# Optimization experiments

Hardware: AMD Instinct MI355X
Metric: run time of the kernel (lower is better)

## Reference

```python
import jax, jax.numpy as jnp
import numpy as np

B, T, D_IN, D_OUT = 4, 2048, 1024, 1024


def setup_inputs() -> dict:
    key = jax.random.key(0)
    k1, k2, k3, k4 = jax.random.split(key, 4)
    s_in = 1.0 / np.sqrt(D_IN)
    return {
        "input_vector": jax.random.normal(k1, (B, T, D_IN), dtype=jnp.float32),
        "w_q": jax.random.normal(k2, (D_IN, D_OUT), dtype=jnp.float32) * s_in,
        "w_k": jax.random.normal(k3, (D_IN, D_OUT), dtype=jnp.float32) * s_in,
        "w_v": jax.random.normal(k4, (D_IN, D_OUT), dtype=jnp.float32) * s_in,
    }


def reference(input_vector, w_q, w_k, w_v):
    # projections: [B, T, D_OUT]
    q = jnp.einsum("btd,de->bte", input_vector, w_q)
    k = jnp.einsum("btd,de->bte", input_vector, w_k)
    v = jnp.einsum("btd,de->bte", input_vector, w_v)

    T_ = q.shape[1]
    # raw scores [B, T, T]
    scores = jnp.einsum("bqd,bkd->bqk", q, k)
    # causal mask (strict upper triangle masked to -inf), applied BEFORE scaling
    # (as in the original; -inf is invariant under the scale anyway)
    causal = jnp.tril(jnp.ones((T_, T_), dtype=bool))  # True = keep
    scores = jnp.where(causal[None, :, :], scores, -jnp.inf)
    scores = scores / jnp.sqrt(jnp.asarray(k.shape[-1], scores.dtype))
    attn = jax.nn.softmax(scores, axis=-1)
    # dropout = 0.0 (eval): identity
    return jnp.einsum("bqk,bkd->bqd", attn, v)
```

## Files before the change

### kernel.cpp

```cpp
#include <hip/hip_runtime.h>
#include <cstdint>
#include <math.h>

typedef unsigned short u16;
typedef __attribute__((ext_vector_type(8))) short short8;
typedef __attribute__((ext_vector_type(16))) float f32x16;

__device__ __forceinline__ u16 f2bf(float f) {
  uint32_t u = __float_as_uint(f);
  u += 0x7FFFu + ((u >> 16) & 1u);
  return (u16)(u >> 16);
}
__device__ __forceinline__ float bf2f(u16 h) {
  return __uint_as_float(((uint32_t)h) << 16);
}

__device__ __forceinline__ void async_ld16(u16* lds, const u16* g) {
  __builtin_amdgcn_global_load_lds((const __attribute__((address_space(1))) uint32_t*)g,
                                   (__attribute__((address_space(3))) uint32_t*)lds,
                                   16, 0, 0);
}

template <bool OUT_BF16, int MODE, bool KLIM>
__global__ __launch_bounds__(256) void gemm_bt(
    const u16* __restrict__ A, int lda, long zsA,
    const u16* __restrict__ B, int ldb, long zsB,
    void* __restrict__ Cv, int ldc, long zsC,
    int K, float scale, int NB)
{
  const int b = blockIdx.x, zb = blockIdx.y;
  int nb, mb;
  if constexpr (MODE == 1) {
    const int u = b & 7, v = b >> 3;
    nb = v & (NB - 1);
    mb = u * ((int)(gridDim.x >> 3) / NB) + (v / NB);
  } else if constexpr (MODE == 2) {
    const int u = b & 7, idx = b >> 3;
    if (idx <= u) { mb = u;      nb = idx; }
    else          { mb = 15 - u; nb = idx - u - 1; }
  } else if constexpr (MODE == 3) {
    const int u = b & 7, idx = b >> 3;
    mb = (idx < 8) ? u : 15 - u;
    nb = idx & 7;
  } else {
    nb = b % NB;
    mb = b / NB;
  }

  A += (long)zb * zsA;
  B += (long)zb * zsB;
  const int m0 = mb * 128, n0 = nb * 128;

  __shared__ __align__(16) u16 lsA[2][128 * 32];
  __shared__ __align__(16) u16 lsB[2][128 * 32];

  const int tid = threadIdx.x;
  const int lane = tid & 63;
  const int wave = tid >> 6;
  const int wr = (wave >> 1) * 64;
  const int wc = (wave & 1) * 64;

  f32x16 acc[2][2];
#pragma unroll
  for (int i = 0; i < 2; ++i)
#pragma unroll
    for (int j = 0; j < 2; ++j)
#pragma unroll
      for (int r = 0; r < 16; ++r) acc[i][j][r] = 0.f;

  const int c0 = tid;
  const int c1 = tid + 256;
  const int r0 = c0 >> 2, q0 = ((c0 & 3) ^ ((c0 >> 3) & 3)) * 8;
  const int r1 = c1 >> 2, q1 = ((c1 & 3) ^ ((c1 >> 3) & 3)) * 8;

  const int klim = (mb + 1) * 128;
  const int kmax = KLIM ? (K < klim ? K : klim) : K;

  const u16* pA0 = A + (long)(m0 + r0) * lda + q0;
  const u16* pA1 = A + (long)(m0 + r1) * lda + q1;
  const u16* pB0 = B + (long)(n0 + r0) * ldb + q0;
  const u16* pB1 = B + (long)(n0 + r1) * ldb + q1;

  const int m32 = lane & 31;
  const int hh = lane >> 5;
  const int rsw = (m32 >> 1) & 3;
  int offA[2][2], offB[2][2];
#pragma unroll
  for (int i = 0; i < 2; ++i)
#pragma unroll
    for (int ks = 0; ks < 2; ++ks) {
      const int kq = ((ks << 1) | hh) ^ rsw;
      offA[i][ks] = (wr + i * 32 + m32) * 32 + kq * 8;
      offB[i][ks] = (wc + i * 32 + m32) * 32 + kq * 8;
    }

  async_ld16(&lsA[0][c0 * 8], pA0);
  async_ld16(&lsA[0][c1 * 8], pA1);
  async_ld16(&lsB[0][c0 * 8], pB0);
  async_ld16(&lsB[0][c1 * 8], pB1);
  pA0 += 32; pA1 += 32; pB0 += 32; pB1 += 32;

  int p = 0;
  for (int k0 = 0; k0 < kmax; k0 += 32) {
    __syncthreads();
    if (k0 + 32 < kmax) {
      async_ld16(&lsA[p ^ 1][c0 * 8], pA0);
      async_ld16(&lsA[p ^ 1][c1 * 8], pA1);
      async_ld16(&lsB[p ^ 1][c0 * 8], pB0);
      async_ld16(&lsB[p ^ 1][c1 * 8], pB1);
      pA0 += 32; pA1 += 32; pB0 += 32; pB1 += 32;
    }

    const u16* la = lsA[p];
    const u16* lb = lsB[p];
#pragma unroll
    for (int ks = 0; ks < 2; ++ks) {
      const short8 a0 = *(const short8*)&la[offA[0][ks]];
      const short8 a1 = *(const short8*)&la[offA[1][ks]];
      const short8 b0 = *(const short8*)&lb[offB[0][ks]];
      const short8 b1 = *(const short8*)&lb[offB[1][ks]];
      acc[0][0] = __builtin_amdgcn_mfma_f32_32x32x16_bf16(a0, b0, acc[0][0], 0, 0, 0);
      acc[0][1] = __builtin_amdgcn_mfma_f32_32x32x16_bf16(a0, b1, acc[0][1], 0, 0, 0);
      acc[1][0] = __builtin_amdgcn_mfma_f32_32x32x16_bf16(a1, b0, acc[1][0], 0, 0, 0);
      acc[1][1] = __builtin_amdgcn_mfma_f32_32x32x16_bf16(a1, b1, acc[1][1], 0, 0, 0);
    }
    p ^= 1;
  }

  const int ec = lane & 31;
  const int rb = (lane >> 5) * 4;

  if constexpr (OUT_BF16) {
    u16* C = (u16*)Cv + (long)zb * zsC;
#pragma unroll
    for (int i = 0; i < 2; ++i) {
      const int rbase = m0 + wr + i * 32 + rb;
#pragma unroll
      for (int j = 0; j < 2; ++j) {
        const int col = n0 + wc + j * 32 + ec;
#pragma unroll
        for (int r = 0; r < 16; ++r) {
          const int row = rbase + (r & 3) + 8 * (r >> 2);
          C[(long)row * ldc + col] = f2bf(acc[i][j][r] * scale);
        }
      }
    }
  } else {
    float* C = (float*)Cv + (long)zb * zsC;
#pragma unroll
    for (int i = 0; i < 2; ++i) {
      const int rbase = m0 + wr + i * 32 + rb;
#pragma unroll
      for (int j = 0; j < 2; ++j) {
        const int col = n0 + wc + j * 32 + ec;
#pragma unroll
        for (int r = 0; r < 16; ++r) {
          const int row = rbase + (r & 3) + 8 * (r >> 2);
          C[(long)row * ldc + col] = acc[i][j][r] * scale;
        }
      }
    }
  }
}

__global__ __launch_bounds__(256) void cast_x_kernel(const float* __restrict__ x,
                                                     u16* __restrict__ y) {
  const long i = ((long)blockIdx.x * 256 + threadIdx.x) * 4;
  const float4 v = *(const float4*)(x + i);
  ushort4 o;
  o.x = f2bf(v.x); o.y = f2bf(v.y); o.z = f2bf(v.z); o.w = f2bf(v.w);
  *(ushort4*)(y + i) = o;
}

__global__ __launch_bounds__(256) void cast_wt_kernel(const float* __restrict__ w0,
                                                      const float* __restrict__ w1,
                                                      const float* __restrict__ w2,
                                                      u16* __restrict__ Wt) {
  const float* W = (blockIdx.z == 0) ? w0 : (blockIdx.z == 1) ? w1 : w2;
  u16* o = Wt + (long)blockIdx.z * 1024 * 1024;
  __shared__ float t[32][33];
  const int n0 = blockIdx.x * 32, k0 = blockIdx.y * 32;
  const int tx = threadIdx.x, ty = threadIdx.y;
  for (int r = ty; r < 32; r += 8) t[r][tx] = W[(long)(k0 + r) * 1024 + n0 + tx];
  __syncthreads();
  for (int r = ty; r < 32; r += 8) o[(long)(n0 + r) * 1024 + k0 + tx] = f2bf(t[tx][r]);
}

__global__ __launch_bounds__(256) void transpose_v_kernel(const u16* __restrict__ V,
                                                          u16* __restrict__ Vt) {
  __shared__ u16 t[32][33];
  const int d0 = blockIdx.x * 32, t0 = blockIdx.y * 32, b = blockIdx.z;
  const u16* Vb = V + (long)b * 2048 * 1024;
  u16* Ob = Vt + (long)b * 1024 * 2048;
  const int tx = threadIdx.x, ty = threadIdx.y;
  for (int r = ty; r < 32; r += 8) t[r][tx] = Vb[(long)(t0 + r) * 1024 + d0 + tx];
  __syncthreads();
  for (int r = ty; r < 32; r += 8) Ob[(long)(d0 + r) * 2048 + t0 + tx] = t[tx][r];
}

__global__ __launch_bounds__(256) void softmax_rows(const u16* __restrict__ S,
                                                    u16* __restrict__ P, int T) {
  const int q = blockIdx.x, b = blockIdx.y;
  const u16* srow = S + ((long)b * T + q) * T;
  u16* prow = P + ((long)b * T + q) * T;
  const int L = q + 1;
  const int Lpad = ((q >> 7) + 1) << 7;
  const int tid = threadIdx.x;

  float sv[8];
  float m = -3.4e38f;
#pragma unroll
  for (int i = 0; i < 8; ++i) {
    const int j = tid + i * 256;
    sv[i] = (j < L) ? bf2f(srow[j]) : -3.4e38f;
    m = fmaxf(m, sv[i]);
  }
#pragma unroll
  for (int off = 32; off > 0; off >>= 1) m = fmaxf(m, __shfl_down(m, off, 64));

  __shared__ float red[4];
  __shared__ float bcast;
  if ((tid & 63) == 0) red[tid >> 6] = m;
  __syncthreads();
  if (tid == 0) bcast = fmaxf(fmaxf(red[0], red[1]), fmaxf(red[2], red[3]));
  __syncthreads();
  m = bcast;

  float s = 0.f;
#pragma unroll
  for (int i = 0; i < 8; ++i) {
    const int j = tid + i * 256;
    sv[i] = (j < L) ? __expf(sv[i] - m) : 0.f;
    s += sv[i];
  }
#pragma unroll
  for (int off = 32; off > 0; off >>= 1) s += __shfl_down(s, off, 64);
  __syncthreads();
  if ((tid & 63) == 0) red[tid >> 6] = s;
  __syncthreads();
  if (tid == 0) bcast = red[0] + red[1] + red[2] + red[3];
  __syncthreads();
  const float inv = 1.f / bcast;

#pragma unroll
  for (int i = 0; i < 8; ++i) {
    const int j = tid + i * 256;
    if (j < Lpad) prow[j] = f2bf(sv[i] * inv);
  }
}

extern "C" void kernel_launch(void* const* d_in, const int* in_sizes, int n_in,
                              void* d_out, int out_size, void* d_ws, size_t ws_size,
                              hipStream_t stream) {
  const float* X  = (const float*)d_in[0];
  const float* Wq = (const float*)d_in[1];
  const float* Wk = (const float*)d_in[2];
  const float* Wv = (const float*)d_in[3];
  float* out = (float*)d_out;

  const long BT = 8192;
  const long Tq = 2048, D = 1024;

  u16* Xbf = (u16*)d_ws;
  u16* Wt  = Xbf + BT * D;
  u16* QKV = Wt + 3 * D * D;
  u16* Vt  = QKV + 3 * BT * D;
  u16* Sb  = Vt + 4 * D * Tq;
  u16* P   = Sb + 4 * Tq * Tq;

  cast_x_kernel<<<8192, 256, 0, stream>>>(X, Xbf);
  cast_wt_kernel<<<dim3(32, 32, 3), dim3(32, 8), 0, stream>>>(Wq, Wk, Wv, Wt);

  gemm_bt<true, 1, false><<<dim3(512, 3), 256, 0, stream>>>(
      Xbf, 1024, 0L, Wt, 1024, D * D, QKV, 1024, BT * D, 1024, 1.0f, 8);

  gemm_bt<true, 2, false><<<dim3(136, 4), 256, 0, stream>>>(
      QKV, 1024, Tq * D, QKV + BT * D, 1024, Tq * D,
      Sb, 2048, Tq * Tq, 1024, 0.03125f, 16);

  softmax_rows<<<dim3(2048, 4), 256, 0, stream>>>(Sb, P, 2048);

  transpose_v_kernel<<<dim3(32, 64, 4), dim3(32, 8), 0, stream>>>(QKV + 2 * BT * D, Vt);

  gemm_bt<false, 3, true><<<dim3(128, 4), 256, 0, stream>>>(
      P, 2048, Tq * Tq, Vt, 2048, D * Tq,
      out, 1024, Tq * D, 2048, 1.0f, 8);
}
```

Measured before the change: 272.8 us.

## Fuse softmax into QK^T epilogue and defer normalization to PV GEMM

```diff
diff --git a/kernel.cpp b/kernel.cpp
--- a/kernel.cpp
+++ b/kernel.cpp
@@ -21,12 +21,12 @@
                                    16, 0, 0);
 }
 
-template <bool OUT_BF16, int MODE, bool KLIM>
+template <int MODE, bool KLIM, int EPI>
 __global__ __launch_bounds__(256) void gemm_bt(
     const u16* __restrict__ A, int lda, long zsA,
     const u16* __restrict__ B, int ldb, long zsB,
     void* __restrict__ Cv, int ldc, long zsC,
-    int K, float scale, int NB)
+    float* __restrict__ l, int K, float scale, int NB)
 {
   const int b = blockIdx.x, zb = blockIdx.y;
   int nb, mb;
@@ -130,7 +130,7 @@
   const int ec = lane & 31;
   const int rb = (lane >> 5) * 4;
 
-  if constexpr (OUT_BF16) {
+  if constexpr (EPI == 1) {
     u16* C = (u16*)Cv + (long)zb * zsC;
 #pragma unroll
     for (int i = 0; i < 2; ++i) {
@@ -145,8 +145,39 @@
         }
       }
     }
+  } else if constexpr (EPI == 2) {
+    u16* C = (u16*)Cv + (long)zb * zsC;
+    float* lz = l + (long)zb * 2048;
+#pragma unroll
+    for (int i = 0; i < 2; ++i) {
+      const int rbase = m0 + wr + i * 32 + rb;
+      float rsum[16];
+#pragma unroll
+      for (int r = 0; r < 16; ++r) rsum[r] = 0.f;
+#pragma unroll
+      for (int j = 0; j < 2; ++j) {
+        const int col = n0 + wc + j * 32 + ec;
+#pragma unroll
+        for (int r = 0; r < 16; ++r) {
+          const int row = rbase + (r & 3) + 8 * (r >> 2);
+          float pv = __expf(acc[i][j][r] * scale);
+          if (col > row) pv = 0.f;
+          C[(long)row * ldc + col] = f2bf(pv);
+          rsum[r] += pv;
+        }
+      }
+#pragma unroll
+      for (int r = 0; r < 16; ++r) {
+        float s = rsum[r];
+#pragma unroll
+        for (int off = 1; off < 32; off <<= 1) s += __shfl_xor(s, off, 64);
+        if ((lane & 31) == 0)
+          atomicAdd(&lz[rbase + (r & 3) + 8 * (r >> 2)], s);
+      }
+    }
   } else {
     float* C = (float*)Cv + (long)zb * zsC;
+    const float* lz = l + (long)zb * 2048;
 #pragma unroll
     for (int i = 0; i < 2; ++i) {
       const int rbase = m0 + wr + i * 32 + rb;
@@ -156,7 +187,7 @@
 #pragma unroll
         for (int r = 0; r < 16; ++r) {
           const int row = rbase + (r & 3) + 8 * (r >> 2);
-          C[(long)row * ldc + col] = acc[i][j][r] * scale;
+          C[(long)row * ldc + col] = acc[i][j][r] / lz[row];
         }
       }
     }
@@ -164,12 +195,19 @@
 }
 
 __global__ __launch_bounds__(256) void cast_x_kernel(const float* __restrict__ x,
-                                                     u16* __restrict__ y) {
+                                                     u16* __restrict__ y,
+                                                     float* __restrict__ l) {
   const long i = ((long)blockIdx.x * 256 + threadIdx.x) * 4;
   const float4 v = *(const float4*)(x + i);
   ushort4 o;
   o.x = f2bf(v.x); o.y = f2bf(v.y); o.z = f2bf(v.z); o.w = f2bf(v.w);
   *(ushort4*)(y + i) = o;
+  if (blockIdx.x == 0) {
+    float4 z = {0.f, 0.f, 0.f, 0.f};
+#pragma unroll
+    for (int k = 0; k < 8; ++k)
+      ((float4*)l)[threadIdx.x * 8 + k] = z;
+  }
 }
 
 __global__ __launch_bounds__(256) void cast_wt_kernel(const float* __restrict__ w0,
@@ -198,57 +236,6 @@
   for (int r = ty; r < 32; r += 8) Ob[(long)(d0 + r) * 2048 + t0 + tx] = t[tx][r];
 }
 
-__global__ __launch_bounds__(256) void softmax_rows(const u16* __restrict__ S,
-                                                    u16* __restrict__ P, int T) {
-  const int q = blockIdx.x, b = blockIdx.y;
-  const u16* srow = S + ((long)b * T + q) * T;
-  u16* prow = P + ((long)b * T + q) * T;
-  const int L = q + 1;
-  const int Lpad = ((q >> 7) + 1) << 7;
-  const int tid = threadIdx.x;
-
-  float sv[8];
-  float m = -3.4e38f;
-#pragma unroll
-  for (int i = 0; i < 8; ++i) {
-    const int j = tid + i * 256;
-    sv[i] = (j < L) ? bf2f(srow[j]) : -3.4e38f;
-    m = fmaxf(m, sv[i]);
-  }
-#pragma unroll
-  for (int off = 32; off > 0; off >>= 1) m = fmaxf(m, __shfl_down(m, off, 64));
-
-  __shared__ float red[4];
-  __shared__ float bcast;
-  if ((tid & 63) == 0) red[tid >> 6] = m;
-  __syncthreads();
-  if (tid == 0) bcast = fmaxf(fmaxf(red[0], red[1]), fmaxf(red[2], red[3]));
-  __syncthreads();
-  m = bcast;
-
-  float s = 0.f;
-#pragma unroll
-  for (int i = 0; i < 8; ++i) {
-    const int j = tid + i * 256;
-    sv[i] = (j < L) ? __expf(sv[i] - m) : 0.f;
-    s += sv[i];
-  }
-#pragma unroll
-  for (int off = 32; off > 0; off >>= 1) s += __shfl_down(s, off, 64);
-  __syncthreads();
-  if ((tid & 63) == 0) red[tid >> 6] = s;
-  __syncthreads();
-  if (tid == 0) bcast = red[0] + red[1] + red[2] + red[3];
-  __syncthreads();
-  const float inv = 1.f / bcast;
-
-#pragma unroll
-  for (int i = 0; i < 8; ++i) {
-    const int j = tid + i * 256;
-    if (j < Lpad) prow[j] = f2bf(sv[i] * inv);
-  }
-}
-
 extern "C" void kernel_launch(void* const* d_in, const int* in_sizes, int n_in,
                               void* d_out, int out_size, void* d_ws, size_t ws_size,
                               hipStream_t stream) {
@@ -265,24 +252,22 @@
   u16* Wt  = Xbf + BT * D;
   u16* QKV = Wt + 3 * D * D;
   u16* Vt  = QKV + 3 * BT * D;
-  u16* Sb  = Vt + 4 * D * Tq;
-  u16* P   = Sb + 4 * Tq * Tq;
-
-  cast_x_kernel<<<8192, 256, 0, stream>>>(X, Xbf);
+  u16* P   = Vt + 4 * D * Tq;
+  float* l = (float*)(P + 4 * Tq * Tq);
+
+  cast_x_kernel<<<8192, 256, 0, stream>>>(X, Xbf, l);
   cast_wt_kernel<<<dim3(32, 32, 3), dim3(32, 8), 0, stream>>>(Wq, Wk, Wv, Wt);
 
-  gemm_bt<true, 1, false><<<dim3(512, 3), 256, 0, stream>>>(
-      Xbf, 1024, 0L, Wt, 1024, D * D, QKV, 1024, BT * D, 1024, 1.0f, 8);
-
-  gemm_bt<true, 2, false><<<dim3(136, 4), 256, 0, stream>>>(
+  gemm_bt<1, false, 1><<<dim3(512, 3), 256, 0, stream>>>(
+      Xbf, 1024, 0L, Wt, 1024, D * D, QKV, 1024, BT * D, nullptr, 1024, 1.0f, 8);
+
+  gemm_bt<2, false, 2><<<dim3(136, 4), 256, 0, stream>>>(
       QKV, 1024, Tq * D, QKV + BT * D, 1024, Tq * D,
-      Sb, 2048, Tq * Tq, 1024, 0.03125f, 16);
-
-  softmax_rows<<<dim3(2048, 4), 256, 0, stream>>>(Sb, P, 2048);
+      P, 2048, Tq * Tq, l, 1024, 0.03125f, 16);
 
   transpose_v_kernel<<<dim3(32, 64, 4), dim3(32, 8), 0, stream>>>(QKV + 2 * BT * D, Vt);
 
-  gemm_bt<false, 3, true><<<dim3(128, 4), 256, 0, stream>>>(
+  gemm_bt<3, true, 3><<<dim3(128, 4), 256, 0, stream>>>(
       P, 2048, Tq * Tq, Vt, 2048, D * Tq,
-      out, 1024, Tq * D, 2048, 1.0f, 8);
-}
+      out, 1024, Tq * D, l, 2048, 1.0f, 8);
+}
```

Result: slower. 283.6 us (+4.0%).
